# Kernel optimization log

Measured on AMD Instinct MI355X. Metric: run time of the kernel, lower is better.

Reference implementation:

```python
import jax, jax.numpy as jnp
import numpy as np

K = 1024          # num_embeddings
D = 64            # embedding_dim
COMMIT = 0.25
DIVERSITY = 0.1


def setup_inputs() -> dict:
    key = jax.random.key(0)
    k1, k2 = jax.random.split(key)
    inputs = jax.random.normal(k1, (64, D, 32, 32), dtype=jnp.float32)
    emb = jax.random.uniform(k2, (K, D), dtype=jnp.float32,
                             minval=-1.0 / K, maxval=1.0 / K)
    return {"inputs": inputs, "emb": emb}


def reference(inputs, emb):
    # NCHW -> NHWC, flatten to [N, D]
    x = jnp.transpose(inputs, (0, 2, 3, 1))          # [B,H,W,D]
    flat = x.reshape(-1, D)                           # [N,D]

    dist = (jnp.sum(flat * flat, axis=1, keepdims=True)
            + jnp.sum(emb * emb, axis=1)
            - 2.0 * flat @ emb.T)
    idx = jnp.argmin(dist, axis=1)                    # [N]
    encodings = jax.nn.one_hot(idx, K, dtype=flat.dtype)  # [N,K]

    # codebook lookup (equivalent to encodings @ emb)
    quantized = jnp.take(emb, idx, axis=0).reshape(x.shape)  # [B,H,W,D]

    sg = jax.lax.stop_gradient
    e_latent_loss = jnp.mean((sg(quantized) - x) ** 2)
    q_latent_loss = jnp.mean((quantized - sg(x)) ** 2)

    avg_probs = jnp.mean(encodings, axis=0)           # [K]
    perplexity = jnp.exp(-jnp.sum(avg_probs * jnp.log(avg_probs + 1e-10)))
    diversity_loss = DIVERSITY * (K - perplexity) / K

    loss = q_latent_loss + COMMIT * e_latent_loss + diversity_loss

    # straight-through estimator
    quantized_st = x + sg(quantized - x)
    quant_out = jnp.transpose(quantized_st, (0, 3, 1, 2))  # NHWC -> NCHW

    return loss, quant_out, perplexity, encodings, idx[:, None]
```

## Files before the change

### kernel.cpp

```cpp
#include <hip/hip_runtime.h>
#include <math.h>

namespace {
constexpr int Kc = 1024;
constexpr int Dd = 64;

__device__ inline float np_sumsq64(const float* __restrict__ a) {
#pragma clang fp contract(off)
    float r[8];
    #pragma unroll
    for (int j = 0; j < 8; ++j) r[j] = a[j] * a[j];
    #pragma unroll
    for (int i = 8; i < 64; i += 8) {
        #pragma unroll
        for (int j = 0; j < 8; ++j) {
            float s = a[i + j] * a[i + j];
            r[j] = r[j] + s;
        }
    }
    return ((r[0] + r[1]) + (r[2] + r[3])) + ((r[4] + r[5]) + (r[6] + r[7]));
}

__global__ void k_ee(const float* __restrict__ emb, float* __restrict__ ee) {
    int k = blockIdx.x * blockDim.x + threadIdx.x;
    ee[k] = np_sumsq64(emb + (size_t)k * Dd);
}

__global__ __launch_bounds__(256, 4) void k_main(
    const float* __restrict__ inputs, const float* __restrict__ emb,
    const float* __restrict__ ee_g, float* __restrict__ quant,
    float* __restrict__ enc, float* __restrict__ idx_out,
    unsigned int* __restrict__ hist, float* __restrict__ partials)
{
    __shared__ float sb[4][64];
    __shared__ int   si[4][64];

    const int tid = threadIdx.x;
    const int p = __builtin_amdgcn_readfirstlane(tid >> 6);
    const int l = tid & 63;
    const int n = blockIdx.x * 64 + l;
    const int b = n >> 10;
    const int hw = n & 1023;

    const float* xin = inputs + (size_t)b * (Dd * 1024) + hw;
    float x[Dd];
    #pragma unroll
    for (int d = 0; d < Dd; ++d) x[d] = xin[d * 1024];

    const float xx = np_sumsq64(x);

    float4* enc4 = (float4*)enc + (size_t)blockIdx.x * 16384 + tid;

    float best = INFINITY;
    int i1 = 0;
    const int k0 = p * 256;
    for (int kk = 0; kk < 256; ++kk) {
        const int k = __builtin_amdgcn_readfirstlane(k0 + kk);
        const float* ek = emb + (size_t)k * Dd;
        float g = 0.f;
        #pragma unroll
        for (int d = 0; d < Dd; ++d) g = fmaf(x[d], ek[d], g);
        float A = xx + ee_g[k];
        float dist = fmaf(-2.f, g, A);
        bool lt = dist < best;
        best = lt ? dist : best;
        i1   = lt ? k    : i1;
        if ((kk & 3) == 0) {
            *enc4 = float4{0.f, 0.f, 0.f, 0.f};
            enc4 += 256;
        }
    }

    sb[p][l] = best; si[p][l] = i1;
    __syncthreads();

    if (tid < 64) {
        best = INFINITY; i1 = 0;
        #pragma unroll
        for (int q = 0; q < 4; ++q) {
            float s = sb[q][l];
            int   i = si[q][l];
            bool lt = s < best;
            best = lt ? s : best;
            i1   = lt ? i : i1;
        }

        {
            const float4* eb = (const float4*)(emb + (size_t)i1 * Dd);
            float* qout = quant + (size_t)b * (Dd * 1024) + hw;
            #pragma unroll
            for (int i = 0; i < Dd / 4; ++i) {
                float4 v = eb[i];
                qout[(i * 4 + 0) * 1024] = v.x;
                qout[(i * 4 + 1) * 1024] = v.y;
                qout[(i * 4 + 2) * 1024] = v.z;
                qout[(i * 4 + 3) * 1024] = v.w;
            }
        }

        idx_out[n] = (float)i1;
        atomicAdd(hist + i1, 1u);

        enc[(size_t)n * Kc + i1] = 1.0f;

        float v = best;
        #pragma unroll
        for (int off = 32; off > 0; off >>= 1) v += __shfl_down(v, off, 64);
        if (l == 0) partials[blockIdx.x] = v;
    }
}

__global__ __launch_bounds__(1024) void k_fin(
    const unsigned int* __restrict__ hist, const float* __restrict__ partials,
    float* __restrict__ loss_out, float* __restrict__ perp_out)
{
    __shared__ double sd[1024];
    int tid = threadIdx.x;
    double p = (double)hist[tid] * (1.0 / 65536.0);
    sd[tid] = p * log(p + 1e-10);
    __syncthreads();
    for (int s = 512; s > 0; s >>= 1) {
        if (tid < s) sd[tid] += sd[tid + s];
        __syncthreads();
    }
    double ent = sd[0];
    __syncthreads();
    sd[tid] = (double)partials[tid];
    __syncthreads();
    for (int s = 512; s > 0; s >>= 1) {
        if (tid < s) sd[tid] += sd[tid + s];
        __syncthreads();
    }
    if (tid == 0) {
        double perp = exp(-ent);
        double mean = sd[0] * (1.0 / 4194304.0);
        double loss = 1.25 * mean + 0.1 * (1024.0 - perp) / 1024.0;
        loss_out[0] = (float)loss;
        perp_out[0] = (float)perp;
    }
}
}

extern "C" void kernel_launch(void* const* d_in, const int* in_sizes, int n_in,
                              void* d_out, int out_size, void* d_ws, size_t ws_size,
                              hipStream_t stream)
{
    const float* inputs = (const float*)d_in[0];
    const float* emb    = (const float*)d_in[1];
    float* out = (float*)d_out;

    float* loss_out = out;
    float* quant    = out + 1;
    float* perp_out = out + 1 + 4194304;
    float* enc      = out + 2 + 4194304;
    float* idx_out  = out + 2 + 4194304 + 67108864;

    unsigned int* hist = (unsigned int*)d_ws;
    float* partials    = (float*)d_ws + 1024;
    float* ee          = (float*)d_ws + 2048;

    hipMemsetAsync(d_ws, 0, 2048 * sizeof(float), stream);
    k_ee<<<Kc / 256, 256, 0, stream>>>(emb, ee);
    k_main<<<65536 / 64, 256, 0, stream>>>(inputs, emb, ee, quant, enc, idx_out, hist, partials);
    k_fin<<<1, 1024, 0, stream>>>(hist, partials, loss_out, perp_out);
}
```

Baseline: 426.3 us.

## Compute VQ distances with fp16 MFMA and exact fp32 rescoring of candidates

Replaces the per-thread fp32 scalar dot-product search with fp16 matrix-core MFMA (16x16x32) over the codebook. Each lane keeps the top-2 candidates per row, and candidates within a margin are rescored exactly in fp32. Rows where the approximation is ambiguous fall back to a full block-wide fp32 search over all 1024 codes. This cuts the compute-bound distance loop, at the cost of extra complexity and a risk of mismatched argmin if the margin does not bound the fp16 error.

After: 491.7 us. 1.15x slower.

```diff
diff --git a/kernel.cpp b/kernel.cpp
--- a/kernel.cpp
+++ b/kernel.cpp
@@ -1,112 +1,207 @@
 #include <hip/hip_runtime.h>
 #include <math.h>
+
+typedef _Float16 half8 __attribute__((ext_vector_type(8)));
+typedef float floatx4 __attribute__((ext_vector_type(4)));
 
 namespace {
 constexpr int Kc = 1024;
 constexpr int Dd = 64;
-
-__device__ inline float np_sumsq64(const float* __restrict__ a) {
+constexpr float MARGIN = 4e-4f;
+
+__device__ inline float np_sumsq64_s(const float* __restrict__ a, int st) {
 #pragma clang fp contract(off)
     float r[8];
     #pragma unroll
-    for (int j = 0; j < 8; ++j) r[j] = a[j] * a[j];
+    for (int j = 0; j < 8; ++j) r[j] = a[j * st] * a[j * st];
     #pragma unroll
     for (int i = 8; i < 64; i += 8) {
         #pragma unroll
         for (int j = 0; j < 8; ++j) {
-            float s = a[i + j] * a[i + j];
+            float s = a[(i + j) * st] * a[(i + j) * st];
             r[j] = r[j] + s;
         }
     }
     return ((r[0] + r[1]) + (r[2] + r[3])) + ((r[4] + r[5]) + (r[6] + r[7]));
 }
 
-__global__ void k_ee(const float* __restrict__ emb, float* __restrict__ ee) {
+__device__ inline float np_dist(const float* __restrict__ x, int xs,
+                                const float* __restrict__ emb, int k,
+                                float xx, float eek) {
+    const float* e = emb + (size_t)k * Dd;
+    float g = 0.f;
+    #pragma unroll
+    for (int d = 0; d < Dd; ++d) g = fmaf(x[d * xs], e[d], g);
+    float A = xx + eek;
+    return fmaf(-2.f, g, A);
+}
+
+__global__ void k_prep(const float* __restrict__ emb, float* __restrict__ ee,
+                       _Float16* __restrict__ emb16) {
     int k = blockIdx.x * blockDim.x + threadIdx.x;
-    ee[k] = np_sumsq64(emb + (size_t)k * Dd);
+    const float* e = emb + (size_t)k * Dd;
+    ee[k] = np_sumsq64_s(e, 1);
+    #pragma unroll
+    for (int d = 0; d < Dd; ++d) emb16[k * Dd + d] = (_Float16)e[d];
 }
 
 __global__ __launch_bounds__(256, 4) void k_main(
     const float* __restrict__ inputs, const float* __restrict__ emb,
-    const float* __restrict__ ee_g, float* __restrict__ quant,
-    float* __restrict__ enc, float* __restrict__ idx_out,
+    const float* __restrict__ ee_g, const _Float16* __restrict__ emb16,
+    float* __restrict__ quant, float* __restrict__ enc, float* __restrict__ idx_out,
     unsigned int* __restrict__ hist, float* __restrict__ partials)
 {
-    __shared__ float sb[4][64];
-    __shared__ int   si[4][64];
+    __shared__ float eeS[Kc];
+    __shared__ float cD[64][16][2];
+    __shared__ int   cI[64][16][2];
+    __shared__ float red[64];
+    __shared__ int   flagged[64];
+    __shared__ int   nflag;
+    __shared__ float fbD[256];
+    __shared__ int   fbI[256];
 
     const int tid = threadIdx.x;
-    const int p = __builtin_amdgcn_readfirstlane(tid >> 6);
-    const int l = tid & 63;
-    const int n = blockIdx.x * 64 + l;
-    const int b = n >> 10;
-    const int hw = n & 1023;
-
-    const float* xin = inputs + (size_t)b * (Dd * 1024) + hw;
-    float x[Dd];
-    #pragma unroll
-    for (int d = 0; d < Dd; ++d) x[d] = xin[d * 1024];
-
-    const float xx = np_sumsq64(x);
+    const int w   = tid >> 6;
+    const int ln  = tid & 63;
+    const int lm  = ln & 15;
+    const int lq  = ln >> 4;
+
+    if (tid == 0) nflag = 0;
+    #pragma unroll
+    for (int i = 0; i < 4; ++i) eeS[tid + i * 256] = ee_g[tid + i * 256];
+
+    const int nA = blockIdx.x * 64 + w * 16 + lm;
+    const float* xA = inputs + (size_t)(nA >> 10) * (Dd * 1024) + (nA & 1023);
+    half8 a0, a1;
+    #pragma unroll
+    for (int j = 0; j < 8; ++j) {
+        a0[j] = (_Float16)xA[(lq * 8 + j) * 1024];
+        a1[j] = (_Float16)xA[(lq * 8 + j + 32) * 1024];
+    }
+
+    __syncthreads();
 
     float4* enc4 = (float4*)enc + (size_t)blockIdx.x * 16384 + tid;
 
-    float best = INFINITY;
-    int i1 = 0;
-    const int k0 = p * 256;
-    for (int kk = 0; kk < 256; ++kk) {
-        const int k = __builtin_amdgcn_readfirstlane(k0 + kk);
-        const float* ek = emb + (size_t)k * Dd;
-        float g = 0.f;
-        #pragma unroll
-        for (int d = 0; d < Dd; ++d) g = fmaf(x[d], ek[d], g);
-        float A = xx + ee_g[k];
-        float dist = fmaf(-2.f, g, A);
-        bool lt = dist < best;
-        best = lt ? dist : best;
-        i1   = lt ? k    : i1;
-        if ((kk & 3) == 0) {
-            *enc4 = float4{0.f, 0.f, 0.f, 0.f};
-            enc4 += 256;
-        }
-    }
-
-    sb[p][l] = best; si[p][l] = i1;
+    float b1[4], b2[4];
+    int   i1[4], i2[4];
+    #pragma unroll
+    for (int r = 0; r < 4; ++r) { b1[r] = INFINITY; b2[r] = INFINITY; i1[r] = 0; i2[r] = 0; }
+
+    for (int t = 0; t < 64; ++t) {
+        const int kn = t * 16 + lm;
+        const half8 bb0 = *(const half8*)(emb16 + kn * Dd + lq * 8);
+        const half8 bb1 = *(const half8*)(emb16 + kn * Dd + 32 + lq * 8);
+        floatx4 acc = {0.f, 0.f, 0.f, 0.f};
+        acc = __builtin_amdgcn_mfma_f32_16x16x32_f16(a0, bb0, acc, 0, 0, 0);
+        acc = __builtin_amdgcn_mfma_f32_16x16x32_f16(a1, bb1, acc, 0, 0, 0);
+        const float eev = eeS[kn];
+        #pragma unroll
+        for (int r = 0; r < 4; ++r) {
+            float s = fmaf(-2.f, acc[r], eev);
+            bool lt1 = s < b1[r], lt2 = s < b2[r];
+            b2[r] = lt1 ? b1[r] : (lt2 ? s : b2[r]);
+            i2[r] = lt1 ? i1[r] : (lt2 ? kn : i2[r]);
+            b1[r] = lt1 ? s : b1[r];
+            i1[r] = lt1 ? kn : i1[r];
+        }
+        *enc4 = float4{0.f, 0.f, 0.f, 0.f};
+        enc4 += 256;
+    }
+
+    #pragma unroll
+    for (int r = 0; r < 4; ++r) {
+        int p = w * 16 + lq * 4 + r;
+        cD[p][lm][0] = b1[r]; cI[p][lm][0] = i1[r];
+        cD[p][lm][1] = b2[r]; cI[p][lm][1] = i2[r];
+    }
     __syncthreads();
 
     if (tid < 64) {
-        best = INFINITY; i1 = 0;
-        #pragma unroll
-        for (int q = 0; q < 4; ++q) {
-            float s = sb[q][l];
-            int   i = si[q][l];
-            bool lt = s < best;
-            best = lt ? s : best;
-            i1   = lt ? i : i1;
-        }
-
-        {
-            const float4* eb = (const float4*)(emb + (size_t)i1 * Dd);
-            float* qout = quant + (size_t)b * (Dd * 1024) + hw;
+        const int p = tid;
+        const int n = blockIdx.x * 64 + p;
+        const float* x = inputs + (size_t)(n >> 10) * (Dd * 1024) + (n & 1023);
+        float amin = INFINITY;
+        #pragma unroll
+        for (int c = 0; c < 16; ++c) amin = fminf(amin, cD[p][c][0]);
+        const float M = amin + MARGIN;
+        bool flag = false;
+        #pragma unroll
+        for (int c = 0; c < 16; ++c) flag |= (cD[p][c][1] <= M);
+        if (flag) {
+            int s = atomicAdd(&nflag, 1);
+            flagged[s] = p;
+        } else {
+            const float xx = np_sumsq64_s(x, 1024);
+            float bd = INFINITY; int bi = 0x7fffffff;
+            for (int c = 0; c < 16; ++c)
+                #pragma unroll
+                for (int s2 = 0; s2 < 2; ++s2)
+                    if (cD[p][c][s2] <= M) {
+                        int k = cI[p][c][s2];
+                        float d = np_dist(x, 1024, emb, k, xx, eeS[k]);
+                        if (d < bd || (d == bd && k < bi)) { bd = d; bi = k; }
+                    }
+            const float4* eb = (const float4*)(emb + (size_t)bi * Dd);
+            float* qout = quant + (size_t)(n >> 10) * (Dd * 1024) + (n & 1023);
             #pragma unroll
-            for (int i = 0; i < Dd / 4; ++i) {
+            for (int i = 0; i < 16; ++i) {
                 float4 v = eb[i];
                 qout[(i * 4 + 0) * 1024] = v.x;
                 qout[(i * 4 + 1) * 1024] = v.y;
                 qout[(i * 4 + 2) * 1024] = v.z;
                 qout[(i * 4 + 3) * 1024] = v.w;
             }
-        }
-
-        idx_out[n] = (float)i1;
-        atomicAdd(hist + i1, 1u);
-
-        enc[(size_t)n * Kc + i1] = 1.0f;
-
-        float v = best;
+            idx_out[n] = (float)bi;
+            atomicAdd(hist + bi, 1u);
+            enc[(size_t)n * Kc + bi] = 1.0f;
+            red[p] = bd;
+        }
+    }
+    __syncthreads();
+
+    const int nf = nflag;
+    for (int f = 0; f < nf; ++f) {
+        const int p = flagged[f];
+        const int n = blockIdx.x * 64 + p;
+        const float* x = inputs + (size_t)(n >> 10) * (Dd * 1024) + (n & 1023);
+        const float xx = np_sumsq64_s(x, 1024);
+        float bd = INFINITY; int bi = 0;
+        #pragma unroll
+        for (int q = 0; q < 4; ++q) {
+            int k = tid * 4 + q;
+            float d = np_dist(x, 1024, emb, k, xx, eeS[k]);
+            bool lt = d < bd;
+            bd = lt ? d : bd; bi = lt ? k : bi;
+        }
+        fbD[tid] = bd; fbI[tid] = bi;
+        __syncthreads();
+        if (tid == 0) {
+            float gd = INFINITY; int gi = 0;
+            for (int tt = 0; tt < 256; ++tt)
+                if (fbD[tt] < gd) { gd = fbD[tt]; gi = fbI[tt]; }
+            const float4* eb = (const float4*)(emb + (size_t)gi * Dd);
+            float* qout = quant + (size_t)(n >> 10) * (Dd * 1024) + (n & 1023);
+            for (int i = 0; i < 16; ++i) {
+                float4 v = eb[i];
+                qout[(i * 4 + 0) * 1024] = v.x;
+                qout[(i * 4 + 1) * 1024] = v.y;
+                qout[(i * 4 + 2) * 1024] = v.z;
+                qout[(i * 4 + 3) * 1024] = v.w;
+            }
+            idx_out[n] = (float)gi;
+            atomicAdd(hist + gi, 1u);
+            enc[(size_t)n * Kc + gi] = 1.0f;
+            red[p] = gd;
+        }
+        __syncthreads();
+    }
+
+    if (tid < 64) {
+        float v = red[tid];
         #pragma unroll
         for (int off = 32; off > 0; off >>= 1) v += __shfl_down(v, off, 64);
-        if (l == 0) partials[blockIdx.x] = v;
+        if (ln == 0) partials[blockIdx.x] = v;
     }
 }
 
@@ -158,9 +253,11 @@
     unsigned int* hist = (unsigned int*)d_ws;
     float* partials    = (float*)d_ws + 1024;
     float* ee          = (float*)d_ws + 2048;
+    _Float16* emb16    = (_Float16*)((float*)d_ws + 3072);
 
     hipMemsetAsync(d_ws, 0, 2048 * sizeof(float), stream);
-    k_ee<<<Kc / 256, 256, 0, stream>>>(emb, ee);
-    k_main<<<65536 / 64, 256, 0, stream>>>(inputs, emb, ee, quant, enc, idx_out, hist, partials);
+    k_prep<<<Kc / 256, 256, 0, stream>>>(emb, ee, emb16);
+    k_main<<<65536 / 64, 256, 0, stream>>>(inputs, emb, ee, emb16,
+                                           quant, enc, idx_out, hist, partials);
     k_fin<<<1, 1024, 0, stream>>>(hist, partials, loss_out, perp_out);
 }
```
